# Optimization experiments

Hardware: AMD Instinct MI355X
Metric: run time of the kernel (lower is better)

Reference implementation:

```python
import jax, jax.numpy as jnp
import numpy as np

N, PAIR, M, D, O, R = 4096, 2, 64, 128, 128, 2
MAX_DEG = 32


def setup_inputs() -> dict:
    key = jax.random.key(0)
    k1, k2, k3, k4, k5, k6 = jax.random.split(key, 6)
    node_features = jax.random.normal(k1, (N, PAIR, M, D), dtype=jnp.float32)
    deg = jax.random.randint(k2, (N,), 0, MAX_DEG, dtype=jnp.int32)
    # per-relation Linear params (stored as [in, out]) and self-loop Linear
    W_r = jax.random.normal(k3, (R, D, O), dtype=jnp.float32) / np.sqrt(D)
    b_r = jax.random.normal(k4, (R, O), dtype=jnp.float32) * 0.01
    W0 = jax.random.normal(k5, (D, O), dtype=jnp.float32) / np.sqrt(D)
    b0 = jax.random.normal(k6, (O,), dtype=jnp.float32) * 0.01
    return {"node_features": node_features, "deg": deg, "W_r": W_r,
            "b_r": b_r, "W0": W0, "b0": b0}


def reference(node_features, deg, W_r, b_r, W0, b0):
    # Original: for each relation r, for each neighbor, adds W_r(x_i);
    # i.e. sum_r deg_i * (x_i @ W_r + b_r) = deg_i * (x_i @ sum_r W_r + sum_r b_r)
    Wsum = W_r.sum(axis=0)          # [D, O]
    bsum = b_r.sum(axis=0)          # [O]
    rel = jnp.einsum('npmd,do->npmo', node_features, Wsum) + bsum
    self_term = jnp.einsum('npmd,do->npmo', node_features, W0) + b0
    d = deg.astype(node_features.dtype)[:, None, None, None]
    h = jax.nn.relu(d * rel + self_term)  # [N, 2, M, O]
    # edge representation: mm(h_i, h_j.T) per entity -> [N, M, M]
    out = jnp.einsum('nmo,nko->nmk', h[:, 0], h[:, 1])
    return out
```

## Files before the change

kernel.cpp:

```cpp
#include <hip/hip_runtime.h>
#include <hip/hip_bf16.h>


typedef __attribute__((ext_vector_type(8))) short bf16x8;
typedef __attribute__((ext_vector_type(4))) float f32x4;

#define RAW_BARRIER() do {                                   \
    asm volatile("s_waitcnt lgkmcnt(0)" ::: "memory");       \
    __builtin_amdgcn_s_barrier();                            \
    __builtin_amdgcn_sched_barrier(0);                       \
} while (0)

__device__ __forceinline__ unsigned int pkbf(float a, float b) {
    union { __hip_bfloat162 h; unsigned int u; } v;
    v.h = __float22bfloat162_rn(float2{a, b});
    return v.u;
}

__global__ __launch_bounds__(256) void build_weights(
    const float* __restrict__ W_r,
    const float* __restrict__ b_r,
    const float* __restrict__ W0,
    const float* __restrict__ b0,
    unsigned short* __restrict__ wfrag,
    float* __restrict__ call)
{
    const int t = blockIdx.x * blockDim.x + threadIdx.x;
    const int d = t >> 11;
    const int r = t & 2047;
    const int k = r >> 4;
    const int o0 = (r & 15) * 8;
    const f32x4* wr0 = (const f32x4*)(W_r + k * 128 + o0);
    const f32x4* wr1 = (const f32x4*)(W_r + 128 * 128 + k * 128 + o0);
    const f32x4* w0p = (const f32x4*)(W0 + k * 128 + o0);
    float w[8];
#pragma unroll
    for (int half = 0; half < 2; ++half) {
        f32x4 a = wr0[half], b = wr1[half], c = w0p[half];
#pragma unroll
        for (int i = 0; i < 4; ++i)
            w[half * 4 + i] = (float)d * (a[i] + b[i]) + c[i];
    }
    const int ct = o0 >> 4;
    const int ks = k >> 5;
    const int lhi = (k >> 3) & 3;
    const int j = k & 7;
    unsigned short* base = wfrag +
        ((((size_t)(d * 8 + ct) * 4 + ks) * 64 + lhi * 16 + (o0 & 15))) * 8 + j;
#pragma unroll
    for (int i = 0; i < 8; ++i) {
        union { float f; unsigned u; } v; v.f = w[i];
        unsigned rr = (v.u + 0x7fffu + ((v.u >> 16) & 1u)) >> 16;
        base[i * 8] = (unsigned short)rr;
    }
    if (t < 32 * 128) {
        int dd = t >> 7, oo = t & 127;
        call[t] = (float)dd * (b_r[oo] + b_r[128 + oo]) + b0[oo];
    }
}

__global__ __launch_bounds__(256) void edge_kernel(
    const float* __restrict__ x,
    const int* __restrict__ deg,
    const unsigned short* __restrict__ wfrag,
    const float* __restrict__ call,
    float* __restrict__ out)
{
    __shared__ char ldsb[66048];

    const int n = blockIdx.x;
    const int tid = threadIdx.x;
    const int wave = tid >> 6;
    const int lane = tid & 63;
    const int l15 = lane & 15;
    const int lhi = lane >> 4;
    const int d = deg[n];

    const float* xn = x + (size_t)n * (2 * 64 * 128);
    const char* wsrc = (const char*)(wfrag + (size_t)d * (8 * 4 * 64 * 8));

#pragma unroll
    for (int i = 0; i < 8; ++i) {
        __builtin_amdgcn_global_load_lds(
            (const __attribute__((address_space(1))) unsigned int*)(wsrc + (size_t)i * 4096 + (size_t)tid * 16),
            (__attribute__((address_space(3))) unsigned int*)(ldsb + i * 4096 + wave * 1024),
            16, 0, 0);
    }
    if (tid < 32) {
        __builtin_amdgcn_global_load_lds(
            (const __attribute__((address_space(1))) unsigned int*)(call + d * 128 + tid * 4),
            (__attribute__((address_space(3))) unsigned int*)(ldsb + 65536),
            16, 0, 0);
    }

    const int rbase = wave * 32;
    const float* r0p = xn + (size_t)(rbase + l15) * 128 + lhi * 8;
    const float* r1p = r0p + (size_t)16 * 128;
    bf16x8 afrag[2][4];
    f32x4 ring[4][2];
#pragma unroll
    for (int u = 0; u < 4; ++u) {
        const f32x4* p = (const f32x4*)(r0p + (u & 3) * 32);
        ring[u][0] = p[0];
        ring[u][1] = p[1];
    }
#pragma unroll
    for (int u = 0; u < 8; ++u) {
        f32x4 a0 = ring[u & 3][0];
        f32x4 a1 = ring[u & 3][1];
        if (u < 4) {
            const f32x4* p = (const f32x4*)(r1p + (u & 3) * 32);
            ring[u & 3][0] = p[0];
            ring[u & 3][1] = p[1];
        }
        union { bf16x8 vv; unsigned int uu[4]; } f;
        f.uu[0] = pkbf(a0.x, a0.y);
        f.uu[1] = pkbf(a0.z, a0.w);
        f.uu[2] = pkbf(a1.x, a1.y);
        f.uu[3] = pkbf(a1.z, a1.w);
        afrag[u >> 2][u & 3] = f.vv;
        __builtin_amdgcn_sched_barrier(0);
    }

    __syncthreads();

#pragma unroll
    for (int ct = 0; ct < 8; ++ct) {
        bf16x8 bfrag[4];
#pragma unroll
        for (int ks = 0; ks < 4; ++ks)
            bfrag[ks] = *(const bf16x8*)(ldsb + ct * 4096 + ks * 1024 + lane * 16);
        f32x4 acc[2] = {{0.f,0.f,0.f,0.f},{0.f,0.f,0.f,0.f}};
#pragma unroll
        for (int ks = 0; ks < 4; ++ks)
#pragma unroll
            for (int rt = 0; rt < 2; ++rt)
                acc[rt] = __builtin_amdgcn_mfma_f32_16x16x32_bf16(bfrag[ks], afrag[rt][ks], acc[rt], 0, 0, 0);
        const f32x4 cc4 = *(const f32x4*)(ldsb + 65536 + ct * 64 + lhi * 16);
#pragma unroll
        for (int rt = 0; rt < 2; ++rt) {
            const int m = rbase + rt * 16 + l15;
            const int slot = ((lhi >> 1) ^ ((m >> 2) & 1));
            float h0v = fmaxf(acc[rt][0] + cc4.x, 0.f);
            float h1v = fmaxf(acc[rt][1] + cc4.y, 0.f);
            float h2v = fmaxf(acc[rt][2] + cc4.z, 0.f);
            float h3v = fmaxf(acc[rt][3] + cc4.w, 0.f);
            union { unsigned int u[2]; unsigned long long ull; } pk;
            pk.u[0] = pkbf(h0v, h1v);
            pk.u[1] = pkbf(h2v, h3v);
            *(unsigned long long*)(ldsb + 32768 + ct * 4096 + m * 32 + slot * 16 + (lhi & 1) * 8) = pk.ull;
        }
    }
    RAW_BARRIER();

    const int mrow = wave * 16 + l15;
    bf16x8 hb[4];
#pragma unroll
    for (int ks = 0; ks < 4; ++ks) {
        const int ct = ks * 2 + (lhi >> 1);
        const int s  = (lhi & 1) ^ ((mrow >> 2) & 1);
        hb[ks] = *(const bf16x8*)(ldsb + 32768 + ct * 4096 + mrow * 32 + s * 16);
    }
    float* outn = out + (size_t)n * 4096;
#pragma unroll
    for (int qt = 0; qt < 4; ++qt) {
        const int qrow = 64 + qt * 16 + l15;
        f32x4 acc = {0.f, 0.f, 0.f, 0.f};
#pragma unroll
        for (int ks = 0; ks < 4; ++ks) {
            const int ct = ks * 2 + (lhi >> 1);
            const int s  = (lhi & 1) ^ ((qrow >> 2) & 1);
            bf16x8 ha = *(const bf16x8*)(ldsb + 32768 + ct * 4096 + qrow * 32 + s * 16);
            acc = __builtin_amdgcn_mfma_f32_16x16x32_bf16(ha, hb[ks], acc, 0, 0, 0);
        }
        __builtin_nontemporal_store(acc, (f32x4*)(outn + mrow * 64 + qt * 16 + lhi * 4));
    }
}

extern "C" void kernel_launch(void* const* d_in, const int* in_sizes, int n_in,
                              void* d_out, int out_size, void* d_ws, size_t ws_size,
                              hipStream_t stream) {
    const float* x   = (const float*)d_in[0];
    const int*   deg = (const int*)d_in[1];
    const float* W_r = (const float*)d_in[2];
    const float* b_r = (const float*)d_in[3];
    const float* W0  = (const float*)d_in[4];
    const float* b0  = (const float*)d_in[5];
    float* out = (float*)d_out;

    unsigned short* wfrag = (unsigned short*)d_ws;
    float* call = (float*)((unsigned short*)d_ws + 32 * 8 * 4 * 64 * 8);

    build_weights<<<256, 256, 0, stream>>>(W_r, b_r, W0, b0, wfrag, call);
    edge_kernel<<<4096, 256, 0, stream>>>(x, deg, wfrag, call, out);
}
```

Measured before the change: 70.81 us.

## Stream weight fragments from global into registers instead of staging in LDS

Drops the global-to-LDS staging of the per-degree weight fragments and bias row. Each wave now loads its B fragments straight from global (L2-resident) into a double-buffered register array, prefetching the next column tile while issuing MFMAs on the current one. This halves LDS use to 32KB, which allows more blocks per CU (launch bounds 4), and removes a block-wide barrier. In exchange, every wave redundantly fetches the same 32KB of weights from global/L2, and the prefetch adds register pressure.

```diff
diff --git a/kernel.cpp b/kernel.cpp
--- a/kernel.cpp
+++ b/kernel.cpp
@@ -59,14 +59,14 @@
     }
 }
 
-__global__ __launch_bounds__(256) void edge_kernel(
+__global__ __launch_bounds__(256, 4) void edge_kernel(
     const float* __restrict__ x,
     const int* __restrict__ deg,
     const unsigned short* __restrict__ wfrag,
     const float* __restrict__ call,
     float* __restrict__ out)
 {
-    __shared__ char ldsb[66048];
+    __shared__ char hlds[32768];
 
     const int n = blockIdx.x;
     const int tid = threadIdx.x;
@@ -77,21 +77,8 @@
     const int d = deg[n];
 
     const float* xn = x + (size_t)n * (2 * 64 * 128);
-    const char* wsrc = (const char*)(wfrag + (size_t)d * (8 * 4 * 64 * 8));
-
-#pragma unroll
-    for (int i = 0; i < 8; ++i) {
-        __builtin_amdgcn_global_load_lds(
-            (const __attribute__((address_space(1))) unsigned int*)(wsrc + (size_t)i * 4096 + (size_t)tid * 16),
-            (__attribute__((address_space(3))) unsigned int*)(ldsb + i * 4096 + wave * 1024),
-            16, 0, 0);
-    }
-    if (tid < 32) {
-        __builtin_amdgcn_global_load_lds(
-            (const __attribute__((address_space(1))) unsigned int*)(call + d * 128 + tid * 4),
-            (__attribute__((address_space(3))) unsigned int*)(ldsb + 65536),
-            16, 0, 0);
-    }
+    const unsigned short* wfd = wfrag + (size_t)d * 16384;
+    const float* cdg = call + d * 128;
 
     const int rbase = wave * 32;
     const float* r0p = xn + (size_t)(rbase + l15) * 128 + lhi * 8;
@@ -104,6 +91,11 @@
         ring[u][0] = p[0];
         ring[u][1] = p[1];
     }
+    bf16x8 wbuf[2][4];
+#pragma unroll
+    for (int ks = 0; ks < 4; ++ks)
+        wbuf[0][ks] = *(const bf16x8*)(wfd + (size_t)ks * 512 + lane * 8);
+
 #pragma unroll
     for (int u = 0; u < 8; ++u) {
         f32x4 a0 = ring[u & 3][0];
@@ -122,21 +114,21 @@
         __builtin_amdgcn_sched_barrier(0);
     }
 
-    __syncthreads();
-
 #pragma unroll
     for (int ct = 0; ct < 8; ++ct) {
-        bf16x8 bfrag[4];
+        if (ct < 7) {
 #pragma unroll
-        for (int ks = 0; ks < 4; ++ks)
-            bfrag[ks] = *(const bf16x8*)(ldsb + ct * 4096 + ks * 1024 + lane * 16);
+            for (int ks = 0; ks < 4; ++ks)
+                wbuf[(ct + 1) & 1][ks] =
+                    *(const bf16x8*)(wfd + (size_t)((ct + 1) * 4 + ks) * 512 + lane * 8);
+        }
+        const f32x4 cc4 = *(const f32x4*)(cdg + ct * 16 + lhi * 4);
         f32x4 acc[2] = {{0.f,0.f,0.f,0.f},{0.f,0.f,0.f,0.f}};
 #pragma unroll
         for (int ks = 0; ks < 4; ++ks)
 #pragma unroll
             for (int rt = 0; rt < 2; ++rt)
-                acc[rt] = __builtin_amdgcn_mfma_f32_16x16x32_bf16(bfrag[ks], afrag[rt][ks], acc[rt], 0, 0, 0);
-        const f32x4 cc4 = *(const f32x4*)(ldsb + 65536 + ct * 64 + lhi * 16);
+                acc[rt] = __builtin_amdgcn_mfma_f32_16x16x32_bf16(wbuf[ct & 1][ks], afrag[rt][ks], acc[rt], 0, 0, 0);
 #pragma unroll
         for (int rt = 0; rt < 2; ++rt) {
             const int m = rbase + rt * 16 + l15;
@@ -148,7 +140,7 @@
             union { unsigned int u[2]; unsigned long long ull; } pk;
             pk.u[0] = pkbf(h0v, h1v);
             pk.u[1] = pkbf(h2v, h3v);
-            *(unsigned long long*)(ldsb + 32768 + ct * 4096 + m * 32 + slot * 16 + (lhi & 1) * 8) = pk.ull;
+            *(unsigned long long*)(hlds + ct * 4096 + m * 32 + slot * 16 + (lhi & 1) * 8) = pk.ull;
         }
     }
     RAW_BARRIER();
@@ -159,7 +151,7 @@
     for (int ks = 0; ks < 4; ++ks) {
         const int ct = ks * 2 + (lhi >> 1);
         const int s  = (lhi & 1) ^ ((mrow >> 2) & 1);
-        hb[ks] = *(const bf16x8*)(ldsb + 32768 + ct * 4096 + mrow * 32 + s * 16);
+        hb[ks] = *(const bf16x8*)(hlds + ct * 4096 + mrow * 32 + s * 16);
     }
     float* outn = out + (size_t)n * 4096;
 #pragma unroll
@@ -170,7 +162,7 @@
         for (int ks = 0; ks < 4; ++ks) {
             const int ct = ks * 2 + (lhi >> 1);
             const int s  = (lhi & 1) ^ ((qrow >> 2) & 1);
-            bf16x8 ha = *(const bf16x8*)(ldsb + 32768 + ct * 4096 + qrow * 32 + s * 16);
+            bf16x8 ha = *(const bf16x8*)(hlds + ct * 4096 + qrow * 32 + s * 16);
             acc = __builtin_amdgcn_mfma_f32_16x16x32_bf16(ha, hb[ks], acc, 0, 0, 0);
         }
         __builtin_nontemporal_store(acc, (f32x4*)(outn + mrow * 64 + qt * 16 + lhi * 4));
```

Result: slower. 73.26 us (+3.5%).
